# Optimization experiments

Hardware: AMD Instinct MI355X
Metric: run time of the kernel (lower is better)

## Reference

```python
import jax, jax.numpy as jnp
import numpy as np

N_USERS = 100000
N_ITEMS = 200000
EMB_DIM = 64
UI_LAYERS = 3
NNZ = 9600000
N_NODES = N_USERS + N_ITEMS


def setup_inputs() -> dict:
    key = jax.random.key(0)
    k1, k2, k3, k4, k5 = jax.random.split(key, 5)
    user_emb = jax.random.normal(k1, (N_USERS, EMB_DIM), dtype=jnp.float32)
    item_emb = jax.random.normal(k2, (N_ITEMS, EMB_DIM), dtype=jnp.float32)
    adj_rows = jax.random.randint(k3, (NNZ,), 0, N_NODES, dtype=jnp.int32)
    adj_cols = jax.random.randint(k4, (NNZ,), 0, N_NODES, dtype=jnp.int32)
    # normalized-adjacency-like small positive values
    adj_vals = jax.random.uniform(k5, (NNZ,), dtype=jnp.float32) * 0.1
    return {"user_emb": user_emb, "item_emb": item_emb,
            "adj_rows": adj_rows, "adj_cols": adj_cols, "adj_vals": adj_vals}


def reference(user_emb, item_emb, adj_rows, adj_cols, adj_vals):
    # ego = cat(user, item) over all N nodes
    ego = jnp.concatenate([user_emb, item_emb], axis=0)  # [N, d]
    acc = ego  # running sum over layer embeddings (layer 0 included)
    for _ in range(UI_LAYERS):
        # SpMM in COO form: out[r] += vals * ego[c]
        gathered = adj_vals[:, None] * ego[adj_cols]  # [nnz, d]
        ego = jax.ops.segment_sum(gathered, adj_rows, num_segments=N_NODES)
        acc = acc + ego
    all_emb = acc / jnp.float32(UI_LAYERS + 1)  # mean over stacked layers
    return all_emb[:N_USERS], all_emb[N_USERS:]
```

## Files before the change

kernel.cpp:

```cpp
#include <hip/hip_runtime.h>

#define N_USERS 100000
#define N_ITEMS 200000
#define N_NODES 300000
#define EMB 64
#define NNZ_C 9600000

#define RPB 256
#define NB 1172
#define NB2 2048
#define P1_CHUNK 9375
#define P2_CHUNK 4096


__global__ void init_kernel(const float4* __restrict__ ue, const float4* __restrict__ ie,
                            float4* __restrict__ ego, float4* __restrict__ acc) {
    const int user4 = N_USERS * EMB / 4;
    const int total4 = N_NODES * EMB / 4;
    int stride = gridDim.x * blockDim.x;
    for (int i = blockIdx.x * blockDim.x + threadIdx.x; i < total4; i += stride) {
        float4 v = (i < user4) ? ue[i] : ie[i - user4];
        ego[i] = v;
        acc[i] = v;
    }
}

__global__ void zero_int_kernel(int* __restrict__ p, int n) {
    int stride = gridDim.x * blockDim.x;
    for (int i = blockIdx.x * blockDim.x + threadIdx.x; i < n; i += stride) p[i] = 0;
}


__global__ __launch_bounds__(1024) void bhist_kernel(const int* __restrict__ rows,
                                                     int* __restrict__ bcounts) {
    __shared__ int lh[NB];
    for (int i = threadIdx.x; i < NB; i += 1024) lh[i] = 0;
    __syncthreads();
    int stride = gridDim.x * blockDim.x;
    for (int e = blockIdx.x * blockDim.x + threadIdx.x; e < NNZ_C; e += stride)
        atomicAdd(&lh[rows[e] >> 8], 1);
    __syncthreads();
    for (int i = threadIdx.x; i < NB; i += 1024)
        if (lh[i]) atomicAdd(&bcounts[i], lh[i]);
}

__global__ __launch_bounds__(1024) void bscan_kernel(const int* __restrict__ bcounts,
                                                     int* __restrict__ bbase,
                                                     int* __restrict__ bcursor) {
    __shared__ int ts[1024];
    int t = threadIdx.x;
    int c0 = (2 * t < NB) ? bcounts[2 * t] : 0;
    int c1 = (2 * t + 1 < NB) ? bcounts[2 * t + 1] : 0;
    int s = c0 + c1;
    ts[t] = s;
    __syncthreads();
    for (int off = 1; off < 1024; off <<= 1) {
        int v = (t >= off) ? ts[t - off] : 0;
        __syncthreads();
        ts[t] += v;
        __syncthreads();
    }
    int excl = ts[t] - s;
    if (2 * t < NB)     { bbase[2 * t] = excl;          bcursor[2 * t] = excl; }
    if (2 * t + 1 < NB) { bbase[2 * t + 1] = excl + c0; bcursor[2 * t + 1] = excl + c0; }
    if (t == 0) bbase[NB] = NNZ_C;
}


__global__ __launch_bounds__(1024) void bin_kernel(const int* __restrict__ rows,
                                                   const int* __restrict__ cols,
                                                   const float* __restrict__ vals,
                                                   int* __restrict__ bcursor,
                                                   uint2* __restrict__ cvt) {
    __shared__ int lh[NB2];
    __shared__ int lb[NB2];
    __shared__ int gb[NB];
    __shared__ int ts[1024];
    __shared__ uint2 stg[P1_CHUNK];
    __shared__ unsigned short sbk[P1_CHUNK];
    int tid = threadIdx.x;
    for (int c = 0; c < 4; ++c) {
        int cb = (blockIdx.x * 4 + c) * P1_CHUNK;
        lh[tid] = 0;
        lh[tid + 1024] = 0;
        __syncthreads();
        int ebr[10]; int epk[10]; float evl[10];
        #pragma unroll
        for (int j = 0; j < 10; ++j) {
            int i = j * 1024 + tid;
            ebr[j] = -1;
            if (i < P1_CHUNK) {
                int e = cb + i;
                int r = rows[e];
                int cc = cols[e];
                float v = vals[e];
                int bk = r >> 8;
                int rk = atomicAdd(&lh[bk], 1);
                ebr[j] = (bk << 14) | rk;
                epk[j] = ((r & 255) << 19) | cc;
                evl[j] = v;
            }
        }
        __syncthreads();
        int c0 = lh[2 * tid], c1 = lh[2 * tid + 1];
        int s = c0 + c1;
        ts[tid] = s;
        __syncthreads();
        for (int off = 1; off < 1024; off <<= 1) {
            int v = (tid >= off) ? ts[tid - off] : 0;
            __syncthreads();
            ts[tid] += v;
            __syncthreads();
        }
        int excl = ts[tid] - s;
        lb[2 * tid] = excl;
        lb[2 * tid + 1] = excl + c0;
        if (2 * tid < NB && c0)     gb[2 * tid]     = atomicAdd(&bcursor[2 * tid], c0);
        if (2 * tid + 1 < NB && c1) gb[2 * tid + 1] = atomicAdd(&bcursor[2 * tid + 1], c1);
        __syncthreads();
        #pragma unroll
        for (int j = 0; j < 10; ++j) {
            if (ebr[j] >= 0) {
                int bk = ebr[j] >> 14, rk = ebr[j] & 16383;
                int idx = lb[bk] + rk;
                stg[idx] = make_uint2((unsigned)epk[j], __float_as_uint(evl[j]));
                sbk[idx] = (unsigned short)bk;
            }
        }
        __syncthreads();
        for (int i = tid; i < P1_CHUNK; i += 1024) {
            int bk = sbk[i];
            int pos = gb[bk] + (i - lb[bk]);
            cvt[pos] = stg[i];
        }
        __syncthreads();
    }
}


__global__ __launch_bounds__(1024) void place_kernel(const int* __restrict__ bbase,
                                                     const uint2* __restrict__ cvt,
                                                     uint2* __restrict__ cv,
                                                     int* __restrict__ row_ptr) {
    __shared__ int cur[RPB];
    __shared__ int lh[RPB];
    __shared__ int lb[RPB];
    __shared__ int sc[RPB];
    __shared__ uint2 stg[P2_CHUNK];
    __shared__ unsigned short srl[P2_CHUNK];
    int b = blockIdx.x, tid = threadIdx.x;
    int beg = bbase[b], end = bbase[b + 1];

    if (tid < RPB) lh[tid] = 0;
    __syncthreads();
    for (int e = beg + tid; e < end; e += 1024)
        atomicAdd(&lh[cvt[e].x >> 19], 1);
    __syncthreads();
    int x = (tid < RPB) ? lh[tid] : 0;
    if (tid < RPB) sc[tid] = x;
    __syncthreads();
    for (int off = 1; off < RPB; off <<= 1) {
        int t = (tid < RPB && tid >= off) ? sc[tid - off] : 0;
        __syncthreads();
        if (tid < RPB) sc[tid] += t;
        __syncthreads();
    }
    if (tid < RPB) {
        int base = beg + sc[tid] - x;
        cur[tid] = base;
        int r = b * RPB + tid;
        if (r < N_NODES) row_ptr[r] = base;
    }
    if (b == 0 && tid == 0) row_ptr[N_NODES] = NNZ_C;
    __syncthreads();

    for (int cb = beg; cb < end; cb += P2_CHUNK) {
        int cnum = min(P2_CHUNK, end - cb);
        if (tid < RPB) lh[tid] = 0;
        __syncthreads();
        uint2 p[4]; int prl[4], prk[4];
        #pragma unroll
        for (int j = 0; j < 4; ++j) {
            int i = j * 1024 + tid;
            prl[j] = -1;
            if (i < cnum) {
                p[j] = cvt[cb + i];
                prl[j] = p[j].x >> 19;
                prk[j] = atomicAdd(&lh[prl[j]], 1);
            }
        }
        __syncthreads();
        int y = (tid < RPB) ? lh[tid] : 0;
        if (tid < RPB) sc[tid] = y;
        __syncthreads();
        for (int off = 1; off < RPB; off <<= 1) {
            int t = (tid < RPB && tid >= off) ? sc[tid - off] : 0;
            __syncthreads();
            if (tid < RPB) sc[tid] += t;
            __syncthreads();
        }
        if (tid < RPB) lb[tid] = sc[tid] - y;
        __syncthreads();
        #pragma unroll
        for (int j = 0; j < 4; ++j) {
            if (prl[j] >= 0) {
                int idx = lb[prl[j]] + prk[j];
                stg[idx] = p[j];
                srl[idx] = (unsigned short)prl[j];
            }
        }
        __syncthreads();
        for (int i = tid; i < cnum; i += 1024) {
            int rl = srl[i];
            int pos = cur[rl] + (i - lb[rl]);
            uint2 q = stg[i];
            cv[pos] = make_uint2(q.x & 0x7FFFF, q.y);
        }
        __syncthreads();
        if (tid < RPB) cur[tid] += lh[tid];
        __syncthreads();
    }
}


__global__ void spmm_seg_kernel(const int* __restrict__ row_ptr, const uint2* __restrict__ cv,
                                const float4* __restrict__ ego_in, float4* __restrict__ ego_out,
                                float4* __restrict__ acc, float scale, int write_ego) {
    int sub = (blockIdx.x * blockDim.x + threadIdx.x) >> 4;
    int lane = threadIdx.x & 15;
    int nsub = (gridDim.x * blockDim.x) >> 4;
    for (int r = sub; r < N_NODES; r += nsub) {
        int beg = row_ptr[r], end = row_ptr[r + 1];
        float4 s0 = make_float4(0.f, 0.f, 0.f, 0.f);
        float4 s1 = make_float4(0.f, 0.f, 0.f, 0.f);
        int e = beg;
        for (; e + 2 <= end; e += 2) {
            uint2 p0 = cv[e];
            uint2 p1 = cv[e + 1];
            float4 x0 = ego_in[p0.x * 16 + lane];
            float4 x1 = ego_in[p1.x * 16 + lane];
            float v0 = __uint_as_float(p0.y);
            float v1 = __uint_as_float(p1.y);
            s0.x += v0 * x0.x; s0.y += v0 * x0.y; s0.z += v0 * x0.z; s0.w += v0 * x0.w;
            s1.x += v1 * x1.x; s1.y += v1 * x1.y; s1.z += v1 * x1.z; s1.w += v1 * x1.w;
        }
        if (e < end) {
            uint2 p0 = cv[e];
            float4 x0 = ego_in[p0.x * 16 + lane];
            float v0 = __uint_as_float(p0.y);
            s0.x += v0 * x0.x; s0.y += v0 * x0.y; s0.z += v0 * x0.z; s0.w += v0 * x0.w;
        }
        float4 s = make_float4(s0.x + s1.x, s0.y + s1.y, s0.z + s1.z, s0.w + s1.w);
        int o = r * 16 + lane;
        float4 a = acc[o];
        a.x = (a.x + s.x) * scale;
        a.y = (a.y + s.y) * scale;
        a.z = (a.z + s.z) * scale;
        a.w = (a.w + s.w) * scale;
        acc[o] = a;
        if (write_ego) ego_out[o] = s;
    }
}


__global__ void zero4_kernel(float4* __restrict__ p, int n4) {
    int stride = gridDim.x * blockDim.x;
    float4 z = make_float4(0.f, 0.f, 0.f, 0.f);
    for (int i = blockIdx.x * blockDim.x + threadIdx.x; i < n4; i += stride) p[i] = z;
}

__global__ void spmm_atomic_kernel(const int* __restrict__ rows, const int* __restrict__ cols,
                                   const float* __restrict__ vals,
                                   const float* __restrict__ ego_in, float* __restrict__ ego_out) {
    int wave = (blockIdx.x * blockDim.x + threadIdx.x) >> 6;
    int lane = threadIdx.x & 63;
    int nwaves = (gridDim.x * blockDim.x) >> 6;
    for (int e = wave; e < NNZ_C; e += nwaves) {
        int r = rows[e];
        int c = cols[e];
        float v = vals[e];
        float x = ego_in[c * EMB + lane];
        atomicAdd(&ego_out[r * EMB + lane], v * x);
    }
}

__global__ void add_kernel(float4* __restrict__ acc, const float4* __restrict__ ego,
                           float scale, int n4) {
    int stride = gridDim.x * blockDim.x;
    for (int i = blockIdx.x * blockDim.x + threadIdx.x; i < n4; i += stride) {
        float4 a = acc[i];
        float4 g = ego[i];
        a.x = (a.x + g.x) * scale;
        a.y = (a.y + g.y) * scale;
        a.z = (a.z + g.z) * scale;
        a.w = (a.w + g.w) * scale;
        acc[i] = a;
    }
}


extern "C" void kernel_launch(void* const* d_in, const int* in_sizes, int n_in,
                              void* d_out, int out_size, void* d_ws, size_t ws_size,
                              hipStream_t stream) {
    const float* user_emb = (const float*)d_in[0];
    const float* item_emb = (const float*)d_in[1];
    const int*   adj_rows = (const int*)d_in[2];
    const int*   adj_cols = (const int*)d_in[3];
    const float* adj_vals = (const float*)d_in[4];
    float* acc = (float*)d_out;

    const size_t egoN = (size_t)N_NODES * EMB;
    float* ego_a = (float*)d_ws;
    float* ego_b = ego_a + egoN;

    const int total4 = N_NODES * EMB / 4;
    const int EW_BLOCKS = 4096, EW_THREADS = 256;

    uint2* cvt     = (uint2*)ego_b;
    uint2* cv      = (uint2*)(ego_b + egoN);
    int* bcounts   = (int*)(cv + (size_t)NNZ_C);
    int* bbase     = bcounts + NB;
    int* bcursor   = bbase + (NB + 1);
    int* row_ptr   = bcursor + NB;
    size_t needed  = (size_t)((char*)(row_ptr + N_NODES + 1) - (char*)d_ws);

    if (ws_size >= needed) {
        zero_int_kernel<<<2, 1024, 0, stream>>>(bcounts, NB);
        bhist_kernel<<<512, 1024, 0, stream>>>(adj_rows, bcounts);
        bscan_kernel<<<1, 1024, 0, stream>>>(bcounts, bbase, bcursor);
        bin_kernel<<<256, 1024, 0, stream>>>(adj_rows, adj_cols, adj_vals, bcursor, cvt);
        place_kernel<<<NB, 1024, 0, stream>>>(bbase, cvt, cv, row_ptr);

        init_kernel<<<EW_BLOCKS, EW_THREADS, 0, stream>>>(
            (const float4*)user_emb, (const float4*)item_emb,
            (float4*)ego_a, (float4*)acc);

        spmm_seg_kernel<<<2048, 256, 0, stream>>>(row_ptr, cv, (const float4*)ego_a,
                                                  (float4*)ego_b, (float4*)acc, 1.0f, 1);
        spmm_seg_kernel<<<2048, 256, 0, stream>>>(row_ptr, cv, (const float4*)ego_b,
                                                  (float4*)ego_a, (float4*)acc, 1.0f, 1);
        spmm_seg_kernel<<<2048, 256, 0, stream>>>(row_ptr, cv, (const float4*)ego_a,
                                                  (float4*)ego_b, (float4*)acc, 0.25f, 0);
    } else {
        init_kernel<<<EW_BLOCKS, EW_THREADS, 0, stream>>>(
            (const float4*)user_emb, (const float4*)item_emb,
            (float4*)ego_a, (float4*)acc);
        float* ego_in = ego_a;
        float* ego_out = ego_b;
        for (int layer = 0; layer < 3; ++layer) {
            zero4_kernel<<<EW_BLOCKS, EW_THREADS, 0, stream>>>((float4*)ego_out, total4);
            spmm_atomic_kernel<<<4096, 256, 0, stream>>>(
                adj_rows, adj_cols, adj_vals, ego_in, ego_out);
            float scale = (layer == 2) ? 0.25f : 1.0f;
            add_kernel<<<EW_BLOCKS, EW_THREADS, 0, stream>>>(
                (float4*)acc, (const float4*)ego_out, scale, total4);
            float* t = ego_in; ego_in = ego_out; ego_out = t;
        }
    }
}
```

Measured before the change: 1.471 ms.

## Remove init pass, read user/item directly, defer layer accumulation to one merge kernel

The SpMM kernel now reads the user and item embeddings directly through two base pointers, so the concat/init pass is no longer needed. Each layer writes only its own output, and a final merge kernel combines the inputs, layer 1 and layer 2 outputs, and the layer 3 output (written into acc), then scales by one quarter. The edge loop is unrolled to four with nontemporal loads of the packed column/value pairs. This cuts the per-layer read-modify-write traffic on acc, at the cost of a branch per gathered row and one extra merge pass.

New measurement: 1.582 ms. 1.08x slower.

```diff
diff --git a/kernel.cpp b/kernel.cpp
--- a/kernel.cpp
+++ b/kernel.cpp
@@ -11,6 +11,8 @@
 #define NB2 2048
 #define P1_CHUNK 9375
 #define P2_CHUNK 4096
+
+typedef __attribute__((ext_vector_type(4))) float f4;
 
 
 __global__ void init_kernel(const float4* __restrict__ ue, const float4* __restrict__ ie,
@@ -223,9 +225,11 @@
 }
 
 
-__global__ void spmm_seg_kernel(const int* __restrict__ row_ptr, const uint2* __restrict__ cv,
-                                const float4* __restrict__ ego_in, float4* __restrict__ ego_out,
-                                float4* __restrict__ acc, float scale, int write_ego) {
+__global__ __launch_bounds__(256) void spmm_seg_kernel(
+        const int* __restrict__ row_ptr, const uint2* __restrict__ cv,
+        const float4* __restrict__ ego_u, const float4* __restrict__ ego_i,
+        float4* __restrict__ ego_out) {
+    const unsigned long long* cvq = (const unsigned long long*)cv;
     int sub = (blockIdx.x * blockDim.x + threadIdx.x) >> 4;
     int lane = threadIdx.x & 15;
     int nsub = (gridDim.x * blockDim.x) >> 4;
@@ -233,32 +237,67 @@
         int beg = row_ptr[r], end = row_ptr[r + 1];
         float4 s0 = make_float4(0.f, 0.f, 0.f, 0.f);
         float4 s1 = make_float4(0.f, 0.f, 0.f, 0.f);
+        float4 s2 = make_float4(0.f, 0.f, 0.f, 0.f);
+        float4 s3 = make_float4(0.f, 0.f, 0.f, 0.f);
         int e = beg;
-        for (; e + 2 <= end; e += 2) {
-            uint2 p0 = cv[e];
-            uint2 p1 = cv[e + 1];
-            float4 x0 = ego_in[p0.x * 16 + lane];
-            float4 x1 = ego_in[p1.x * 16 + lane];
-            float v0 = __uint_as_float(p0.y);
-            float v1 = __uint_as_float(p1.y);
+        for (; e + 4 <= end; e += 4) {
+            unsigned long long q0 = __builtin_nontemporal_load(cvq + e);
+            unsigned long long q1 = __builtin_nontemporal_load(cvq + e + 1);
+            unsigned long long q2 = __builtin_nontemporal_load(cvq + e + 2);
+            unsigned long long q3 = __builtin_nontemporal_load(cvq + e + 3);
+            unsigned c0 = (unsigned)q0, c1 = (unsigned)q1;
+            unsigned c2 = (unsigned)q2, c3 = (unsigned)q3;
+            const float4* b0 = (c0 < N_USERS) ? ego_u + (size_t)c0 * 16 : ego_i + ((size_t)c0 - N_USERS) * 16;
+            const float4* b1 = (c1 < N_USERS) ? ego_u + (size_t)c1 * 16 : ego_i + ((size_t)c1 - N_USERS) * 16;
+            const float4* b2 = (c2 < N_USERS) ? ego_u + (size_t)c2 * 16 : ego_i + ((size_t)c2 - N_USERS) * 16;
+            const float4* b3 = (c3 < N_USERS) ? ego_u + (size_t)c3 * 16 : ego_i + ((size_t)c3 - N_USERS) * 16;
+            float4 x0 = b0[lane];
+            float4 x1 = b1[lane];
+            float4 x2 = b2[lane];
+            float4 x3 = b3[lane];
+            float v0 = __uint_as_float((unsigned)(q0 >> 32));
+            float v1 = __uint_as_float((unsigned)(q1 >> 32));
+            float v2 = __uint_as_float((unsigned)(q2 >> 32));
+            float v3 = __uint_as_float((unsigned)(q3 >> 32));
             s0.x += v0 * x0.x; s0.y += v0 * x0.y; s0.z += v0 * x0.z; s0.w += v0 * x0.w;
             s1.x += v1 * x1.x; s1.y += v1 * x1.y; s1.z += v1 * x1.z; s1.w += v1 * x1.w;
-        }
-        if (e < end) {
-            uint2 p0 = cv[e];
-            float4 x0 = ego_in[p0.x * 16 + lane];
-            float v0 = __uint_as_float(p0.y);
+            s2.x += v2 * x2.x; s2.y += v2 * x2.y; s2.z += v2 * x2.z; s2.w += v2 * x2.w;
+            s3.x += v3 * x3.x; s3.y += v3 * x3.y; s3.z += v3 * x3.z; s3.w += v3 * x3.w;
+        }
+        for (; e < end; ++e) {
+            unsigned long long q0 = __builtin_nontemporal_load(cvq + e);
+            unsigned c0 = (unsigned)q0;
+            const float4* b0 = (c0 < N_USERS) ? ego_u + (size_t)c0 * 16 : ego_i + ((size_t)c0 - N_USERS) * 16;
+            float4 x0 = b0[lane];
+            float v0 = __uint_as_float((unsigned)(q0 >> 32));
             s0.x += v0 * x0.x; s0.y += v0 * x0.y; s0.z += v0 * x0.z; s0.w += v0 * x0.w;
         }
-        float4 s = make_float4(s0.x + s1.x, s0.y + s1.y, s0.z + s1.z, s0.w + s1.w);
-        int o = r * 16 + lane;
-        float4 a = acc[o];
-        a.x = (a.x + s.x) * scale;
-        a.y = (a.y + s.y) * scale;
-        a.z = (a.z + s.z) * scale;
-        a.w = (a.w + s.w) * scale;
-        acc[o] = a;
-        if (write_ego) ego_out[o] = s;
+        float4 s;
+        s.x = (s0.x + s1.x) + (s2.x + s3.x);
+        s.y = (s0.y + s1.y) + (s2.y + s3.y);
+        s.z = (s0.z + s1.z) + (s2.z + s3.z);
+        s.w = (s0.w + s1.w) + (s2.w + s3.w);
+        ego_out[r * 16 + lane] = s;
+    }
+}
+
+
+__global__ __launch_bounds__(256) void merge_kernel(const f4* __restrict__ ue,
+                                                    const f4* __restrict__ ie,
+                                                    const f4* __restrict__ e1,
+                                                    const f4* __restrict__ e2,
+                                                    f4* __restrict__ acc) {
+    const int user4 = N_USERS * EMB / 4;
+    const int total4 = N_NODES * EMB / 4;
+    int stride = gridDim.x * blockDim.x;
+    for (int i = blockIdx.x * blockDim.x + threadIdx.x; i < total4; i += stride) {
+        f4 v0 = (i < user4) ? __builtin_nontemporal_load(ue + i)
+                            : __builtin_nontemporal_load(ie + (i - user4));
+        f4 a = __builtin_nontemporal_load(e1 + i);
+        f4 b = __builtin_nontemporal_load(e2 + i);
+        f4 c = acc[i];
+        f4 o = (((v0 + a) + b) + c) * 0.25f;
+        __builtin_nontemporal_store(o, acc + i);
     }
 }
 
@@ -331,16 +370,22 @@
         bin_kernel<<<256, 1024, 0, stream>>>(adj_rows, adj_cols, adj_vals, bcursor, cvt);
         place_kernel<<<NB, 1024, 0, stream>>>(bbase, cvt, cv, row_ptr);
 
-        init_kernel<<<EW_BLOCKS, EW_THREADS, 0, stream>>>(
-            (const float4*)user_emb, (const float4*)item_emb,
-            (float4*)ego_a, (float4*)acc);
-
-        spmm_seg_kernel<<<2048, 256, 0, stream>>>(row_ptr, cv, (const float4*)ego_a,
-                                                  (float4*)ego_b, (float4*)acc, 1.0f, 1);
-        spmm_seg_kernel<<<2048, 256, 0, stream>>>(row_ptr, cv, (const float4*)ego_b,
-                                                  (float4*)ego_a, (float4*)acc, 1.0f, 1);
-        spmm_seg_kernel<<<2048, 256, 0, stream>>>(row_ptr, cv, (const float4*)ego_a,
-                                                  (float4*)ego_b, (float4*)acc, 0.25f, 0);
+        const float4* ue4 = (const float4*)user_emb;
+        const float4* ie4 = (const float4*)item_emb;
+        float4* A = (float4*)ego_a;
+        float4* B = (float4*)ego_b;
+
+        spmm_seg_kernel<<<2048, 256, 0, stream>>>(row_ptr, cv, ue4, ie4, A);
+        spmm_seg_kernel<<<2048, 256, 0, stream>>>(row_ptr, cv,
+                                                  (const float4*)A,
+                                                  (const float4*)(A + (size_t)N_USERS * 16), B);
+        spmm_seg_kernel<<<2048, 256, 0, stream>>>(row_ptr, cv,
+                                                  (const float4*)B,
+                                                  (const float4*)(B + (size_t)N_USERS * 16),
+                                                  (float4*)acc);
+        merge_kernel<<<EW_BLOCKS, EW_THREADS, 0, stream>>>(
+            (const f4*)user_emb, (const f4*)item_emb,
+            (const f4*)ego_a, (const f4*)ego_b, (f4*)acc);
     } else {
         init_kernel<<<EW_BLOCKS, EW_THREADS, 0, stream>>>(
             (const float4*)user_emb, (const float4*)item_emb,
```

## Split embedding dimension into halves to shrink gather working set

Applied to the files above, without the earlier changes.

The SpMM now runs in two passes over 32-column halves of the embedding, each stored as a compact plane, so every gather touches 128 bytes per row and the randomly accessed source fits better in cache. The first layer reads user and item embeddings directly, which removes the init copy, and a merge kernel builds the layer sum before the last layer fuses the final accumulate and scale. The unroll goes from 2 to 4 edges. The cost is that the edge list (cv) is streamed six times instead of three.

Result: slower. 1.573 ms (+6.9%).

```diff
diff --git a/kernel.cpp b/kernel.cpp
--- a/kernel.cpp
+++ b/kernel.cpp
@@ -223,42 +223,103 @@
 }
 
 
-__global__ void spmm_seg_kernel(const int* __restrict__ row_ptr, const uint2* __restrict__ cv,
-                                const float4* __restrict__ ego_in, float4* __restrict__ ego_out,
-                                float4* __restrict__ acc, float scale, int write_ego) {
-    int sub = (blockIdx.x * blockDim.x + threadIdx.x) >> 4;
-    int lane = threadIdx.x & 15;
-    int nsub = (gridDim.x * blockDim.x) >> 4;
+template<int MODE>
+__global__ __launch_bounds__(256) void spmm_half_kernel(
+        const int* __restrict__ row_ptr, const uint2* __restrict__ cv,
+        const float4* __restrict__ srcA, const float4* __restrict__ srcB,
+        float4* __restrict__ outp, int half) {
+    int sub = (blockIdx.x * blockDim.x + threadIdx.x) >> 3;
+    int lane = threadIdx.x & 7;
+    int nsub = (gridDim.x * blockDim.x) >> 3;
+    const int h8 = half * 8;
     for (int r = sub; r < N_NODES; r += nsub) {
         int beg = row_ptr[r], end = row_ptr[r + 1];
         float4 s0 = make_float4(0.f, 0.f, 0.f, 0.f);
         float4 s1 = make_float4(0.f, 0.f, 0.f, 0.f);
+        float4 s2 = make_float4(0.f, 0.f, 0.f, 0.f);
+        float4 s3 = make_float4(0.f, 0.f, 0.f, 0.f);
         int e = beg;
-        for (; e + 2 <= end; e += 2) {
+        for (; e + 4 <= end; e += 4) {
             uint2 p0 = cv[e];
             uint2 p1 = cv[e + 1];
-            float4 x0 = ego_in[p0.x * 16 + lane];
-            float4 x1 = ego_in[p1.x * 16 + lane];
+            uint2 p2 = cv[e + 2];
+            uint2 p3 = cv[e + 3];
+            const float4 *b0, *b1, *b2, *b3;
+            if (MODE == 0) {
+                b0 = (p0.x < N_USERS) ? srcA + (size_t)p0.x * 16 + h8 : srcB + ((size_t)p0.x - N_USERS) * 16 + h8;
+                b1 = (p1.x < N_USERS) ? srcA + (size_t)p1.x * 16 + h8 : srcB + ((size_t)p1.x - N_USERS) * 16 + h8;
+                b2 = (p2.x < N_USERS) ? srcA + (size_t)p2.x * 16 + h8 : srcB + ((size_t)p2.x - N_USERS) * 16 + h8;
+                b3 = (p3.x < N_USERS) ? srcA + (size_t)p3.x * 16 + h8 : srcB + ((size_t)p3.x - N_USERS) * 16 + h8;
+            } else {
+                b0 = srcA + (size_t)p0.x * 8;
+                b1 = srcA + (size_t)p1.x * 8;
+                b2 = srcA + (size_t)p2.x * 8;
+                b3 = srcA + (size_t)p3.x * 8;
+            }
+            float4 x0 = b0[lane];
+            float4 x1 = b1[lane];
+            float4 x2 = b2[lane];
+            float4 x3 = b3[lane];
             float v0 = __uint_as_float(p0.y);
             float v1 = __uint_as_float(p1.y);
+            float v2 = __uint_as_float(p2.y);
+            float v3 = __uint_as_float(p3.y);
             s0.x += v0 * x0.x; s0.y += v0 * x0.y; s0.z += v0 * x0.z; s0.w += v0 * x0.w;
             s1.x += v1 * x1.x; s1.y += v1 * x1.y; s1.z += v1 * x1.z; s1.w += v1 * x1.w;
-        }
-        if (e < end) {
+            s2.x += v2 * x2.x; s2.y += v2 * x2.y; s2.z += v2 * x2.z; s2.w += v2 * x2.w;
+            s3.x += v3 * x3.x; s3.y += v3 * x3.y; s3.z += v3 * x3.z; s3.w += v3 * x3.w;
+        }
+        for (; e < end; ++e) {
             uint2 p0 = cv[e];
-            float4 x0 = ego_in[p0.x * 16 + lane];
+            const float4* b0;
+            if (MODE == 0) {
+                b0 = (p0.x < N_USERS) ? srcA + (size_t)p0.x * 16 + h8 : srcB + ((size_t)p0.x - N_USERS) * 16 + h8;
+            } else {
+                b0 = srcA + (size_t)p0.x * 8;
+            }
+            float4 x0 = b0[lane];
             float v0 = __uint_as_float(p0.y);
             s0.x += v0 * x0.x; s0.y += v0 * x0.y; s0.z += v0 * x0.z; s0.w += v0 * x0.w;
         }
-        float4 s = make_float4(s0.x + s1.x, s0.y + s1.y, s0.z + s1.z, s0.w + s1.w);
-        int o = r * 16 + lane;
-        float4 a = acc[o];
-        a.x = (a.x + s.x) * scale;
-        a.y = (a.y + s.y) * scale;
-        a.z = (a.z + s.z) * scale;
-        a.w = (a.w + s.w) * scale;
-        acc[o] = a;
-        if (write_ego) ego_out[o] = s;
+        float4 s;
+        s.x = (s0.x + s1.x) + (s2.x + s3.x);
+        s.y = (s0.y + s1.y) + (s2.y + s3.y);
+        s.z = (s0.z + s1.z) + (s2.z + s3.z);
+        s.w = (s0.w + s1.w) + (s2.w + s3.w);
+        if (MODE == 2) {
+            int o = r * 16 + h8 + lane;
+            float4 a = outp[o];
+            s.x = (a.x + s.x) * 0.25f;
+            s.y = (a.y + s.y) * 0.25f;
+            s.z = (a.z + s.z) * 0.25f;
+            s.w = (a.w + s.w) * 0.25f;
+            outp[o] = s;
+        } else {
+            outp[r * 8 + lane] = s;
+        }
+    }
+}
+
+
+__global__ __launch_bounds__(256) void mergeh_kernel(const float4* __restrict__ ue,
+                                                     const float4* __restrict__ ie,
+                                                     const float4* __restrict__ e1h,
+                                                     const float4* __restrict__ e2h,
+                                                     float4* __restrict__ acc, int half) {
+    const int user4 = N_USERS * 16;
+    const int totalh = N_NODES * 8;
+    int stride = gridDim.x * blockDim.x;
+    for (int k = blockIdx.x * blockDim.x + threadIdx.x; k < totalh; k += stride) {
+        int n = k >> 3, j = k & 7;
+        int o = n * 16 + half * 8 + j;
+        float4 v = (o < user4) ? ue[o] : ie[o - user4];
+        float4 a = e1h[k];
+        float4 b = e2h[k];
+        v.x += a.x + b.x;
+        v.y += a.y + b.y;
+        v.z += a.z + b.z;
+        v.w += a.w + b.w;
+        acc[o] = v;
     }
 }
 
@@ -331,16 +392,23 @@
         bin_kernel<<<256, 1024, 0, stream>>>(adj_rows, adj_cols, adj_vals, bcursor, cvt);
         place_kernel<<<NB, 1024, 0, stream>>>(bbase, cvt, cv, row_ptr);
 
-        init_kernel<<<EW_BLOCKS, EW_THREADS, 0, stream>>>(
-            (const float4*)user_emb, (const float4*)item_emb,
-            (float4*)ego_a, (float4*)acc);
-
-        spmm_seg_kernel<<<2048, 256, 0, stream>>>(row_ptr, cv, (const float4*)ego_a,
-                                                  (float4*)ego_b, (float4*)acc, 1.0f, 1);
-        spmm_seg_kernel<<<2048, 256, 0, stream>>>(row_ptr, cv, (const float4*)ego_b,
-                                                  (float4*)ego_a, (float4*)acc, 1.0f, 1);
-        spmm_seg_kernel<<<2048, 256, 0, stream>>>(row_ptr, cv, (const float4*)ego_a,
-                                                  (float4*)ego_b, (float4*)acc, 0.25f, 0);
+        const float4* ue4 = (const float4*)user_emb;
+        const float4* ie4 = (const float4*)item_emb;
+        const size_t planeF4 = (size_t)N_NODES * 8;
+
+        for (int h = 0; h < 2; ++h) {
+            float4* e1h = (float4*)ego_a + h * planeF4;
+            float4* e2h = (float4*)ego_b + h * planeF4;
+            spmm_half_kernel<0><<<2048, 256, 0, stream>>>(row_ptr, cv, ue4, ie4, e1h, h);
+            spmm_half_kernel<1><<<2048, 256, 0, stream>>>(row_ptr, cv,
+                                                          (const float4*)e1h, nullptr, e2h, h);
+            mergeh_kernel<<<2048, 256, 0, stream>>>(ue4, ie4,
+                                                    (const float4*)e1h, (const float4*)e2h,
+                                                    (float4*)acc, h);
+            spmm_half_kernel<2><<<2048, 256, 0, stream>>>(row_ptr, cv,
+                                                          (const float4*)e2h, nullptr,
+                                                          (float4*)acc, h);
+        }
     } else {
         init_kernel<<<EW_BLOCKS, EW_THREADS, 0, stream>>>(
             (const float4*)user_emb, (const float4*)item_emb,
```
